# Kernel optimization log

Hardware: AMD Instinct MI355X
Metric: run time of the kernel (lower is better)

## Reference

```python
import jax, jax.numpy as jnp
import numpy as np
from jax.scipy.linalg import expm

B, S, D = 8, 2048, 1024          # batch, seq, input_dim
C, CD = 16, 64                   # num_concepts, concept_dim
L = C * CD                       # latent_dim = 1024
ALPHA, BETA = 0.3, 1.0
LN_EPS = 1e-5                    # torch nn.LayerNorm default


def layer_norm(x, g, b):
    m = jnp.mean(x, axis=-1, keepdims=True)
    v = jnp.mean(jnp.square(x - m), axis=-1, keepdims=True)
    return (x - m) * jax.lax.rsqrt(v + LN_EPS) * g + b


def setup_inputs() -> dict:
    key = jax.random.key(0)
    ks = jax.random.split(key, 8)
    sc = 0.02
    return {
        "x": jax.random.normal(ks[0], (B, S, D), jnp.float32),
        # encoder: Linear(D, 2L) + LayerNorm(2L)
        "enc_w": jax.random.normal(ks[1], (2 * L, D), jnp.float32) * sc,
        "enc_b": jnp.zeros((2 * L,), jnp.float32),
        "enc_g": jnp.ones((2 * L,), jnp.float32),
        "enc_bt": jnp.zeros((2 * L,), jnp.float32),
        # DAG weights [C, C] (torch inits zeros; use small random for non-trivial math)
        "dag_w": jax.random.normal(ks[2], (C, C), jnp.float32) * 0.1,
        # per-concept transforms: Linear(CD,CD) -> LN(CD) -> ReLU -> Linear(CD,CD), stacked over C
        "cw1": jax.random.normal(ks[3], (C, CD, CD), jnp.float32) * sc,
        "cb1": jnp.zeros((C, CD), jnp.float32),
        "cg": jnp.ones((C, CD), jnp.float32),
        "cbt": jnp.zeros((C, CD), jnp.float32),
        "cw2": jax.random.normal(ks[4], (C, CD, CD), jnp.float32) * sc,
        "cb2": jnp.zeros((C, CD), jnp.float32),
        # decoder: Linear(L,L) -> LN(L) -> ReLU -> Linear(L,D)
        "dec_w1": jax.random.normal(ks[5], (L, L), jnp.float32) * sc,
        "dec_b1": jnp.zeros((L,), jnp.float32),
        "dec_g": jnp.ones((L,), jnp.float32),
        "dec_bt": jnp.zeros((L,), jnp.float32),
        "dec_w2": jax.random.normal(ks[6], (D, L), jnp.float32) * sc,
        "dec_b2": jnp.zeros((D,), jnp.float32),
    }


def reference(x, enc_w, enc_b, enc_g, enc_bt, dag_w, cw1, cb1, cg, cbt, cw2, cb2,
              dec_w1, dec_b1, dec_g, dec_bt, dec_w2, dec_b2):
    # ---- encode ----
    h = layer_norm(jnp.einsum('bsd,kd->bsk', x, enc_w) + enc_b, enc_g, enc_bt)  # [B,S,2L]
    mu, logvar = jnp.split(h, 2, axis=-1)                                        # [B,S,L] each
    z = mu  # eval-mode reparameterize

    # ---- causal transform ----
    zc = z.reshape(B, S, C, CD)                                   # [B,S,C,CD]
    dag = jnp.tril(jax.nn.softplus(dag_w), k=-1)                  # [C,C]
    z_causal = zc + jnp.einsum('ij,bsjd->bsid', dag, zc)          # [B,S,C,CD]

    # per-concept Linear -> LN -> ReLU -> Linear, batched over concept axis
    t = jnp.einsum('bsce,cde->bscd', z_causal, cw1) + cb1         # [B,S,C,CD]
    t = layer_norm(t, cg, cbt)
    t = jax.nn.relu(t)
    t = jnp.einsum('bsce,cde->bscd', t, cw2) + cb2
    z_t = t.reshape(B, S, L)

    # ---- decode ----
    d = layer_norm(jnp.einsum('bsl,kl->bsk', z_t, dec_w1) + dec_b1, dec_g, dec_bt)
    d = jax.nn.relu(d)
    x_recon = jnp.einsum('bsl,dl->bsd', d, dec_w2) + dec_b2        # [B,S,D]

    # ---- losses ----
    recon_loss = jnp.mean(jnp.square(x_recon - x))
    kl_loss = -0.5 * jnp.mean(1.0 + logvar - jnp.square(mu) - jnp.exp(logvar))
    dag_loss = jnp.sum(jnp.abs(dag)) + jnp.trace(expm(dag))
    total_loss = recon_loss + ALPHA * kl_loss + BETA * dag_loss
    return x_recon, total_loss, kl_loss, recon_loss, dag_loss
```

## Files before the change

kernel.cpp:

```cpp
#include <hip/hip_runtime.h>
#include <stdint.h>


#define NTOK   16384
#define DIM    1024
#define NC     16
#define CD     64
#define NOUT_ELEMS 16777216

typedef float f32x4 __attribute__((ext_vector_type(4)));
typedef __bf16 bf16x8 __attribute__((ext_vector_type(8)));
typedef unsigned short u16x4 __attribute__((ext_vector_type(4)));
typedef unsigned short u16x8 __attribute__((ext_vector_type(8)));

__device__ float g_scal[3];
__device__ float g_part[512];

__device__ __forceinline__ float b2f(uint16_t u) {
  union { uint32_t i; float f; } v; v.i = ((uint32_t)u) << 16; return v.f;
}
__device__ __forceinline__ uint16_t f2b(float f) {
  union { float f; uint32_t i; } v; v.f = f;
  uint32_t x = v.i;
  return (uint16_t)((x + 0x7fffu + ((x >> 16) & 1u)) >> 16);
}

__device__ __forceinline__ void gload_lds16(const uint16_t* g, uint16_t* l) {
  __builtin_amdgcn_global_load_lds(
      (const __attribute__((address_space(1))) void*)g,
      (__attribute__((address_space(3))) void*)l, 16, 0, 0);
}

__device__ __forceinline__ void cvt8(const float* s, uint16_t* d) {
  const f32x4 a = *(const f32x4*)s;
  const f32x4 b = *(const f32x4*)(s + 4);
  u16x8 o;
  o[0]=f2b(a[0]); o[1]=f2b(a[1]); o[2]=f2b(a[2]); o[3]=f2b(a[3]);
  o[4]=f2b(b[0]); o[5]=f2b(b[1]); o[6]=f2b(b[2]); o[7]=f2b(b[3]);
  *(u16x8*)d = o;
}

__global__ __launch_bounds__(256) void cvt_x_kernel(
    const float* __restrict__ src, uint16_t* __restrict__ dst)
{
  const int i = blockIdx.x * 256 + threadIdx.x;
  cvt8(src + (size_t)i * 8, dst + (size_t)i * 8);
}

__global__ __launch_bounds__(256) void cvt_weights_kernel(
    const float* __restrict__ ew, const float* __restrict__ d1,
    const float* __restrict__ d2, const float* __restrict__ c1,
    const float* __restrict__ c2, uint16_t* __restrict__ out)
{
  const int i = blockIdx.x * 256 + threadIdx.x;
  const float* src; uint16_t* dst; int off;
  if (i < 262144)      { src = ew; dst = out;           off = i; }
  else if (i < 393216) { src = d1; dst = out + 2097152; off = i - 262144; }
  else if (i < 524288) { src = d2; dst = out + 3145728; off = i - 393216; }
  else if (i < 532480) { src = c1; dst = out + 4194304; off = i - 524288; }
  else                 { src = c2; dst = out + 4259840; off = i - 532480; }
  cvt8(src + (size_t)off * 8, dst + (size_t)off * 8);
}

__device__ __forceinline__ void stage_half(
    const uint16_t* __restrict__ G, uint16_t* L, int h, int lda,
    int sr, int pc, int wave)
{
#pragma unroll
  for (int i = 0; i < 2; ++i) {
    const int r = h * 128 + i * 64 + sr;
    gload_lds16(G + (size_t)r * lda + (size_t)((pc ^ (sr & 7)) * 8),
                (uint16_t*)((char*)L + h * 16384 + i * 8192 + wave * 1024));
  }
}

template<typename TC, bool SPLIT, bool RECON>
__global__ __launch_bounds__(512, 2) void gemm256_kernel(
    const uint16_t* __restrict__ A, const uint16_t* __restrict__ Wm,
    const float* __restrict__ bias, TC* __restrict__ C0, TC* __restrict__ C1,
    const float* __restrict__ Xref,
    int K, int lda, int ldw, int ldc)
{
  __shared__ __align__(16) uint16_t lds[65536];

  const int tid  = threadIdx.x;
  const int wave = tid >> 6;
  const int lane = tid & 63;
  const int q    = lane >> 4;
  const int r16  = lane & 15;
  const int wm   = wave >> 2;
  const int wn   = wave & 3;
  const int sr   = tid >> 3;
  const int pc   = tid & 7;

  const int gx  = gridDim.x;
  const int gy  = gridDim.y;
  const int nwg = gx * gy;
  const int o   = blockIdx.y * gx + blockIdx.x;
  const int w   = (o & 7) * (nwg >> 3) + (o >> 3);
  const int bn  = (w & (gy - 1)) * 256;
  const int bm  = (w >> __builtin_ctz(gy)) * 256;

  const uint16_t* Ab = A  + (size_t)bm * lda;
  const uint16_t* Wb = Wm + (size_t)bn * ldw;

  const int T = K >> 6;

  stage_half(Ab,      lds,                 0, lda, sr, pc, wave);
  stage_half(Ab,      lds,                 1, lda, sr, pc, wave);
  stage_half(Wb,      lds + 16384,         0, ldw, sr, pc, wave);
  stage_half(Wb,      lds + 16384,         1, ldw, sr, pc, wave);
  if (T > 1) {
    stage_half(Wb + 64, lds + 32768 + 16384, 0, ldw, sr, pc, wave);
    stage_half(Wb + 64, lds + 32768 + 16384, 1, ldw, sr, pc, wave);
    asm volatile("s_waitcnt vmcnt(4)" ::: "memory");
  } else {
    asm volatile("s_waitcnt vmcnt(0)" ::: "memory");
  }
  __builtin_amdgcn_s_barrier();

  f32x4 acc[8][4] = {};
  const int cxa = r16 & 7;
  const int c0  = (q ^ cxa) * 8;
  const int c1  = ((4 + q) ^ cxa) * 8;

  for (int t = 0; t < T; ++t) {
    uint16_t* As  = lds + (t & 1) * 32768;
    uint16_t* Bs  = As + 16384;
    uint16_t* Asn = lds + ((t & 1) ^ 1) * 32768;

    const uint16_t* a_rd = As + (wm * 128 + r16) * 64;
    const uint16_t* b_rd = Bs + (wn * 64  + r16) * 64;

    bf16x8 bfr[4][2], af0[2][2];
#pragma unroll
    for (int ni = 0; ni < 4; ++ni) {
      bfr[ni][0] = *(const bf16x8*)(b_rd + ni * 1024 + c0);
      bfr[ni][1] = *(const bf16x8*)(b_rd + ni * 1024 + c1);
    }
#pragma unroll
    for (int mi2 = 0; mi2 < 2; ++mi2) {
      af0[mi2][0] = *(const bf16x8*)(a_rd + mi2 * 1024 + c0);
      af0[mi2][1] = *(const bf16x8*)(a_rd + mi2 * 1024 + c1);
    }
    if (t + 1 < T) {
      stage_half(Ab + (size_t)(t + 1) * 64, Asn, 0, lda, sr, pc, wave);
      stage_half(Ab + (size_t)(t + 1) * 64, Asn, 1, lda, sr, pc, wave);
    }
    asm volatile("s_waitcnt lgkmcnt(0)" ::: "memory");
    __builtin_amdgcn_s_barrier();
    if (t + 2 < T) {
      stage_half(Wb + (size_t)(t + 2) * 64, Bs, 0, ldw, sr, pc, wave);
      stage_half(Wb + (size_t)(t + 2) * 64, Bs, 1, ldw, sr, pc, wave);
    }

    __builtin_amdgcn_s_setprio(1);
#pragma unroll
    for (int ks = 0; ks < 2; ++ks)
#pragma unroll
      for (int mi2 = 0; mi2 < 2; ++mi2)
#pragma unroll
        for (int ni = 0; ni < 4; ++ni)
          acc[mi2][ni] = __builtin_amdgcn_mfma_f32_16x16x32_bf16(
              af0[mi2][ks], bfr[ni][ks], acc[mi2][ni], 0, 0, 0);

    bf16x8 aP0 = *(const bf16x8*)(a_rd + 2 * 1024 + c0);
    bf16x8 aP1 = *(const bf16x8*)(a_rd + 2 * 1024 + c1);
#pragma unroll
    for (int mi = 2; mi < 8; ++mi) {
      const bf16x8 a0 = aP0, a1 = aP1;
      if (mi < 7) {
        aP0 = *(const bf16x8*)(a_rd + (mi + 1) * 1024 + c0);
        aP1 = *(const bf16x8*)(a_rd + (mi + 1) * 1024 + c1);
      }
#pragma unroll
      for (int ni = 0; ni < 4; ++ni)
        acc[mi][ni] = __builtin_amdgcn_mfma_f32_16x16x32_bf16(
            a0, bfr[ni][0], acc[mi][ni], 0, 0, 0);
#pragma unroll
      for (int ni = 0; ni < 4; ++ni)
        acc[mi][ni] = __builtin_amdgcn_mfma_f32_16x16x32_bf16(
            a1, bfr[ni][1], acc[mi][ni], 0, 0, 0);
    }
    __builtin_amdgcn_s_setprio(0);

    if (t + 2 < T)      asm volatile("s_waitcnt vmcnt(4)" ::: "memory");
    else if (t + 1 < T) asm volatile("s_waitcnt vmcnt(0)" ::: "memory");
    __builtin_amdgcn_s_barrier();
  }

  TC* Cq = C0;
  int cb = bn;
  if constexpr (SPLIT) {
    if (bn >= 1024) { Cq = C1; cb = bn - 1024; }
  }
  float bv[4];
#pragma unroll
  for (int ni = 0; ni < 4; ++ni) bv[ni] = bias[bn + wn * 64 + ni * 16 + r16];

  float rsum = 0.f;
#pragma unroll
  for (int mi = 0; mi < 8; ++mi) {
    const int rbase = bm + wm * 128 + mi * 16 + q * 4;
#pragma unroll
    for (int r = 0; r < 4; ++r) {
      const size_t rowoff = (size_t)(rbase + r) * ldc + cb;
#pragma unroll
      for (int ni = 0; ni < 4; ++ni) {
        const int loc = wn * 64 + ni * 16 + r16;
        const float v = acc[mi][ni][r] + bv[ni];
        if constexpr (sizeof(TC) == 2)
          Cq[rowoff + loc] = f2b(v);
        else
          Cq[rowoff + loc] = v;
        if constexpr (RECON) {
          const float dd = v - Xref[rowoff + loc];
          rsum += dd * dd;
        }
      }
    }
  }
  if constexpr (RECON) {
#pragma unroll
    for (int m = 1; m < 64; m <<= 1) rsum += __shfl_xor(rsum, m);
    __shared__ float redR[8];
    if (lane == 0) redR[wave] = rsum;
    __syncthreads();
    if (tid == 0) {
      float s = 0.f;
#pragma unroll
      for (int w2 = 0; w2 < 8; ++w2) s += redR[w2];
      atomicAdd(&g_part[256 + (w & 255)], s);
    }
  }
}

__global__ __launch_bounds__(256) void concept_fused_kernel(
    uint16_t* __restrict__ z, const uint16_t* __restrict__ c1b,
    const uint16_t* __restrict__ c2b, const float* __restrict__ cb1,
    const float* __restrict__ cg, const float* __restrict__ cbt,
    const float* __restrict__ cb2)
{
  __shared__ __align__(16) uint16_t Az[128 * 64];
  __shared__ __align__(16) uint16_t W1s[64 * 64];
  __shared__ __align__(16) uint16_t W2s[64 * 64];

  const int tid  = threadIdx.x;
  const int wave = tid >> 6;
  const int lane = tid & 63;
  const int q    = lane >> 4;
  const int r16  = lane & 15;
  const int c    = blockIdx.y;
  const int m0   = blockIdx.x * 128;

  const int lr = tid >> 3;
  const int pc = tid & 7;

#pragma unroll
  for (int i = 0; i < 4; ++i) {
    const int r = i * 32 + lr;
    const int gc = pc ^ (r & 7);
    gload_lds16(z + (size_t)(m0 + r) * DIM + c * 64 + gc * 8,
                (uint16_t*)((char*)Az + i * 4096 + wave * 1024));
  }
#pragma unroll
  for (int i = 0; i < 2; ++i) {
    const int r = i * 32 + lr;
    const int gc = pc ^ (r & 7);
    gload_lds16(c1b + (size_t)c * 4096 + r * 64 + gc * 8,
                (uint16_t*)((char*)W1s + i * 4096 + wave * 1024));
    gload_lds16(c2b + (size_t)c * 4096 + r * 64 + gc * 8,
                (uint16_t*)((char*)W2s + i * 4096 + wave * 1024));
  }
  __syncthreads();

  f32x4 acc[2][4] = {};
#pragma unroll
  for (int ks = 0; ks < 2; ++ks) {
    bf16x8 af[2], wf[4];
#pragma unroll
    for (int mi = 0; mi < 2; ++mi) {
      const int row = wave * 32 + mi * 16 + r16;
      af[mi] = *(const bf16x8*)(Az + row * 64 + ((ks * 4 + q) ^ (row & 7)) * 8);
    }
#pragma unroll
    for (int ni = 0; ni < 4; ++ni) {
      const int d = ni * 16 + r16;
      wf[ni] = *(const bf16x8*)(W1s + d * 64 + ((ks * 4 + q) ^ (d & 7)) * 8);
    }
#pragma unroll
    for (int mi = 0; mi < 2; ++mi)
#pragma unroll
      for (int ni = 0; ni < 4; ++ni)
        acc[mi][ni] = __builtin_amdgcn_mfma_f32_16x16x32_bf16(
            af[mi], wf[ni], acc[mi][ni], 0, 0, 0);
  }

  float b1v[4], cgv[4], cbv[4], b2v[4];
#pragma unroll
  for (int ni = 0; ni < 4; ++ni) {
    const int cn = ni * 16 + r16;
    b1v[ni] = cb1[c * 64 + cn];
    cgv[ni] = cg[c * 64 + cn];
    cbv[ni] = cbt[c * 64 + cn];
    b2v[ni] = cb2[c * 64 + cn];
  }
#pragma unroll
  for (int mi = 0; mi < 2; ++mi) {
#pragma unroll
    for (int r = 0; r < 4; ++r) {
      float s1 = 0.f, s2 = 0.f;
#pragma unroll
      for (int ni = 0; ni < 4; ++ni) {
        const float v = acc[mi][ni][r] + b1v[ni];
        acc[mi][ni][r] = v;
        s1 += v; s2 += v * v;
      }
#pragma unroll
      for (int m = 1; m < 16; m <<= 1) {
        s1 += __shfl_xor(s1, m);
        s2 += __shfl_xor(s2, m);
      }
      const float mean = s1 * (1.f / 64.f);
      const float var  = s2 * (1.f / 64.f) - mean * mean;
      const float rs   = rsqrtf(var + 1e-5f);
      const int row = wave * 32 + mi * 16 + q * 4 + r;
#pragma unroll
      for (int ni = 0; ni < 4; ++ni) {
        const float y = fmaxf((acc[mi][ni][r] - mean) * rs * cgv[ni] + cbv[ni], 0.f);
        const int cn = ni * 16 + r16;
        Az[row * 64 + (((cn >> 3) ^ (row & 7)) * 8) + (cn & 7)] = f2b(y);
      }
    }
  }
  __syncthreads();

  f32x4 acc2[2][4] = {};
#pragma unroll
  for (int ks = 0; ks < 2; ++ks) {
    bf16x8 af[2], wf[4];
#pragma unroll
    for (int mi = 0; mi < 2; ++mi) {
      const int row = wave * 32 + mi * 16 + r16;
      af[mi] = *(const bf16x8*)(Az + row * 64 + ((ks * 4 + q) ^ (row & 7)) * 8);
    }
#pragma unroll
    for (int ni = 0; ni < 4; ++ni) {
      const int d = ni * 16 + r16;
      wf[ni] = *(const bf16x8*)(W2s + d * 64 + ((ks * 4 + q) ^ (d & 7)) * 8);
    }
#pragma unroll
    for (int mi = 0; mi < 2; ++mi)
#pragma unroll
      for (int ni = 0; ni < 4; ++ni)
        acc2[mi][ni] = __builtin_amdgcn_mfma_f32_16x16x32_bf16(
            af[mi], wf[ni], acc2[mi][ni], 0, 0, 0);
  }

#pragma unroll
  for (int mi = 0; mi < 2; ++mi)
#pragma unroll
    for (int ni = 0; ni < 4; ++ni) {
      const int cn = ni * 16 + r16;
#pragma unroll
      for (int r = 0; r < 4; ++r) {
        const int row = wave * 32 + mi * 16 + q * 4 + r;
        z[(size_t)(m0 + row) * DIM + c * 64 + cn] = f2b(acc2[mi][ni][r] + b2v[ni]);
      }
    }
}

__global__ __launch_bounds__(256) void kl_causal_kernel(
    const uint16_t* __restrict__ lv, uint16_t* __restrict__ mu,
    const float* __restrict__ g, const float* __restrict__ b,
    const float* __restrict__ dag_w)
{
  __shared__ __align__(16) float zsh[1024];
  __shared__ float dg[256];
  __shared__ float red[8];
  __shared__ float red2[4];
  const int tid = threadIdx.x;
  const int tok = blockIdx.x;
  const int e0  = tid * 4;

  {
    const int di = tid >> 4, dj = tid & 15;
    dg[tid] = (dj < di) ? log1pf(expf(dag_w[tid])) : 0.f;
  }

  const uint16_t* lvp = lv + (size_t)tok * 1024;
  uint16_t*       mup = mu + (size_t)tok * 1024;

  const u16x4 m4 = *(const u16x4*)(mup + e0);
  const u16x4 l4 = *(const u16x4*)(lvp + e0);
  float xm[4], xl[4];
  float s1 = 0.f, s2 = 0.f;
#pragma unroll
  for (int k = 0; k < 4; ++k) {
    xm[k] = b2f(m4[k]);
    xl[k] = b2f(l4[k]);
    s1 += xm[k] + xl[k];
    s2 += xm[k] * xm[k] + xl[k] * xl[k];
  }
#pragma unroll
  for (int m = 1; m < 64; m <<= 1) {
    s1 += __shfl_xor(s1, m);
    s2 += __shfl_xor(s2, m);
  }
  const int wave = tid >> 6, lane = tid & 63;
  if (lane == 0) { red[wave] = s1; red[4 + wave] = s2; }
  __syncthreads();
  s1 = red[0] + red[1] + red[2] + red[3];
  s2 = red[4] + red[5] + red[6] + red[7];
  const float mean = s1 * (1.f / 2048.f);
  const float var  = s2 * (1.f / 2048.f) - mean * mean;
  const float rs   = rsqrtf(var + 1e-5f);

  const f32x4 g4m = *(const f32x4*)(g + e0);
  const f32x4 b4m = *(const f32x4*)(b + e0);
  const f32x4 g4l = *(const f32x4*)(g + 1024 + e0);
  const f32x4 b4l = *(const f32x4*)(b + 1024 + e0);
  float kl = 0.f;
  f32x4 z;
#pragma unroll
  for (int k = 0; k < 4; ++k) {
    z[k] = (xm[k] - mean) * rs * g4m[k] + b4m[k];
    const float y = (xl[k] - mean) * rs * g4l[k] + b4l[k];
    kl += 1.f + y - z[k] * z[k] - expf(y);
  }
  *(f32x4*)(zsh + e0) = z;
#pragma unroll
  for (int m = 1; m < 64; m <<= 1) kl += __shfl_xor(kl, m);
  if (lane == 0) red2[wave] = kl;
  __syncthreads();
  if (tid == 0)
    atomicAdd(&g_part[tok & 255], red2[0] + red2[1] + red2[2] + red2[3]);

  const int i  = e0 >> 6;
  const int d0 = e0 & 63;
  f32x4 s = *(const f32x4*)(zsh + e0);
  for (int j = 0; j < i; ++j) {
    const float w = dg[i * 16 + j];
    const f32x4 zj = *(const f32x4*)(zsh + j * 64 + d0);
    s[0] += w * zj[0]; s[1] += w * zj[1]; s[2] += w * zj[2]; s[3] += w * zj[3];
  }
  u16x4 o;
#pragma unroll
  for (int k = 0; k < 4; ++k) o[k] = f2b(s[k]);
  *(u16x4*)(mup + e0) = o;
}

__global__ __launch_bounds__(256) void ln_relu_kernel(
    uint16_t* __restrict__ data, const float* __restrict__ g,
    const float* __restrict__ b)
{
  const int tid = threadIdx.x;
  const int e0  = tid * 4;
  uint16_t* p = data + (size_t)blockIdx.x * 1024;

  const u16x4 v4 = *(const u16x4*)(p + e0);
  float x[4];
  float s1 = 0.f, s2 = 0.f;
#pragma unroll
  for (int k = 0; k < 4; ++k) {
    x[k] = b2f(v4[k]);
    s1 += x[k];
    s2 += x[k] * x[k];
  }
#pragma unroll
  for (int m = 1; m < 64; m <<= 1) {
    s1 += __shfl_xor(s1, m);
    s2 += __shfl_xor(s2, m);
  }
  __shared__ float red[8];
  const int wave = tid >> 6, lane = tid & 63;
  if (lane == 0) { red[wave] = s1; red[4 + wave] = s2; }
  __syncthreads();
  s1 = red[0] + red[1] + red[2] + red[3];
  s2 = red[4] + red[5] + red[6] + red[7];
  const float mean = s1 * (1.f / 1024.f);
  const float var  = s2 * (1.f / 1024.f) - mean * mean;
  const float rs   = rsqrtf(var + 1e-5f);

  const f32x4 g4 = *(const f32x4*)(g + e0);
  const f32x4 b4 = *(const f32x4*)(b + e0);
  u16x4 o;
#pragma unroll
  for (int k = 0; k < 4; ++k) {
    const float y = (x[k] - mean) * rs * g4[k] + b4[k];
    o[k] = f2b(fmaxf(y, 0.f));
  }
  *(u16x4*)(p + e0) = o;
}

__global__ __launch_bounds__(256) void dag_init_kernel(
    const float* __restrict__ dag_w)
{
  const int t = threadIdx.x;
  g_part[t] = 0.f;
  g_part[256 + t] = 0.f;
  const int i = t >> 4, j = t & 15;
  const float v = (j < i) ? log1pf(expf(dag_w[t])) : 0.f;
  float s = v;
#pragma unroll
  for (int m = 1; m < 64; m <<= 1) s += __shfl_xor(s, m);
  __shared__ float red[4];
  const int wave = t >> 6, lane = t & 63;
  if (lane == 0) red[wave] = s;
  __syncthreads();
  if (t == 0)
    g_scal[2] = red[0] + red[1] + red[2] + red[3] + 16.f;
}

__global__ __launch_bounds__(256) void finalize_kernel(float* __restrict__ out_tail)
{
  const int tid = threadIdx.x;
  float kl = g_part[tid];
  float rc = g_part[256 + tid];
#pragma unroll
  for (int m = 1; m < 64; m <<= 1) {
    kl += __shfl_xor(kl, m);
    rc += __shfl_xor(rc, m);
  }
  __shared__ float red[8];
  const int wave = tid >> 6, lane = tid & 63;
  if (lane == 0) { red[wave] = kl; red[4 + wave] = rc; }
  __syncthreads();
  if (tid == 0) {
    const float kls = red[0] + red[1] + red[2] + red[3];
    const float rcs = red[4] + red[5] + red[6] + red[7];
    const float kl_l   = -0.5f * kls * (1.f / (16384.f * 1024.f));
    const float recon  = rcs * (1.f / 16777216.f);
    const float dagl   = g_scal[2];
    out_tail[0] = recon + 0.3f * kl_l + 1.0f * dagl;
    out_tail[1] = kl_l;
    out_tail[2] = recon;
    out_tail[3] = dagl;
  }
}

extern "C" void kernel_launch(void* const* d_in, const int* in_sizes, int n_in,
                              void* d_out, int out_size, void* d_ws, size_t ws_size,
                              hipStream_t stream) {
  const float* x      = (const float*)d_in[0];
  const float* enc_w  = (const float*)d_in[1];
  const float* enc_b  = (const float*)d_in[2];
  const float* enc_g  = (const float*)d_in[3];
  const float* enc_bt = (const float*)d_in[4];
  const float* dag_w  = (const float*)d_in[5];
  const float* cw1    = (const float*)d_in[6];
  const float* cb1    = (const float*)d_in[7];
  const float* cg     = (const float*)d_in[8];
  const float* cbt    = (const float*)d_in[9];
  const float* cw2    = (const float*)d_in[10];
  const float* cb2    = (const float*)d_in[11];
  const float* dec_w1 = (const float*)d_in[12];
  const float* dec_b1 = (const float*)d_in[13];
  const float* dec_g  = (const float*)d_in[14];
  const float* dec_bt = (const float*)d_in[15];
  const float* dec_w2 = (const float*)d_in[16];
  const float* dec_b2 = (const float*)d_in[17];

  uint16_t* S    = (uint16_t*)d_ws;
  uint16_t* Wbf  = (uint16_t*)((char*)d_ws + (size_t)NTOK * DIM * 2);
  uint16_t* ewb  = Wbf;
  uint16_t* d1b  = Wbf + 2097152;
  uint16_t* d2b  = Wbf + 3145728;
  uint16_t* c1b  = Wbf + 4194304;
  uint16_t* c2b  = Wbf + 4259840;

  uint16_t* Obf  = (uint16_t*)d_out;
  uint16_t* xbf  = Obf + (size_t)NOUT_ELEMS;
  float*    O    = (float*)d_out;

  dag_init_kernel<<<1, 256, 0, stream>>>(dag_w);

  cvt_x_kernel<<<NOUT_ELEMS / 8 / 256, 256, 0, stream>>>(x, xbf);
  cvt_weights_kernel<<<2112, 256, 0, stream>>>(enc_w, dec_w1, dec_w2, cw1, cw2, Wbf);

  gemm256_kernel<uint16_t, true, false>
      <<<dim3(64, 8, 1), 512, 0, stream>>>(
      xbf, ewb, enc_b, Obf, S, nullptr, DIM, DIM, DIM, DIM);

  kl_causal_kernel<<<NTOK, 256, 0, stream>>>(S, Obf, enc_g, enc_bt, dag_w);

  concept_fused_kernel<<<dim3(128, 16, 1), 256, 0, stream>>>(
      Obf, c1b, c2b, cb1, cg, cbt, cb2);

  gemm256_kernel<uint16_t, false, false>
      <<<dim3(64, 4, 1), 512, 0, stream>>>(
      Obf, d1b, dec_b1, S, S, nullptr, DIM, DIM, DIM, DIM);

  ln_relu_kernel<<<NTOK, 256, 0, stream>>>(S, dec_g, dec_bt);

  gemm256_kernel<float, false, true>
      <<<dim3(64, 4, 1), 512, 0, stream>>>(
      S, d2b, dec_b2, O, O, x, DIM, DIM, DIM, DIM);

  finalize_kernel<<<1, 256, 0, stream>>>(O + (size_t)NOUT_ELEMS);
}
```

Baseline: 383.0 us.

## Fuse x fp32-to-bf16 conversion into encoder GEMM A-tile staging

The encoder GEMM now reads fp32 x directly, converting to bf16 in registers and writing LDS, which removes the separate cvt_x pass and its bf16 round trip through memory. The dag_init kernel is folded into an extra block of the weight conversion kernel to save a launch. The GEMM pipeline also changes: A and B for the next step are both prefetched at the top of each iteration into the other buffer, replacing the two-deep B prefetch and the mid-iteration barrier. The fp32 A path doubles the A global read bytes and adds conversion and register pressure, and the new schedule exposes more load latency per step in all three GEMMs.

```diff
diff --git a/kernel.cpp b/kernel.cpp
--- a/kernel.cpp
+++ b/kernel.cpp
@@ -40,18 +40,29 @@
   *(u16x8*)d = o;
 }
 
-__global__ __launch_bounds__(256) void cvt_x_kernel(
-    const float* __restrict__ src, uint16_t* __restrict__ dst)
-{
-  const int i = blockIdx.x * 256 + threadIdx.x;
-  cvt8(src + (size_t)i * 8, dst + (size_t)i * 8);
-}
-
 __global__ __launch_bounds__(256) void cvt_weights_kernel(
     const float* __restrict__ ew, const float* __restrict__ d1,
     const float* __restrict__ d2, const float* __restrict__ c1,
-    const float* __restrict__ c2, uint16_t* __restrict__ out)
+    const float* __restrict__ c2, uint16_t* __restrict__ out,
+    const float* __restrict__ dag_w)
 {
+  if (blockIdx.x == 2112) {
+    const int t = threadIdx.x;
+    g_part[t] = 0.f;
+    g_part[256 + t] = 0.f;
+    const int i2 = t >> 4, j2 = t & 15;
+    const float v = (j2 < i2) ? log1pf(expf(dag_w[t])) : 0.f;
+    float s = v;
+#pragma unroll
+    for (int m = 1; m < 64; m <<= 1) s += __shfl_xor(s, m);
+    __shared__ float red[4];
+    const int wave = t >> 6, lane = t & 63;
+    if (lane == 0) red[wave] = s;
+    __syncthreads();
+    if (t == 0)
+      g_scal[2] = red[0] + red[1] + red[2] + red[3] + 16.f;
+    return;
+  }
   const int i = blockIdx.x * 256 + threadIdx.x;
   const float* src; uint16_t* dst; int off;
   if (i < 262144)      { src = ew; dst = out;           off = i; }
@@ -74,13 +85,14 @@
   }
 }
 
-template<typename TC, bool SPLIT, bool RECON>
+template<typename TA, typename TC, bool SPLIT, bool RECON>
 __global__ __launch_bounds__(512, 2) void gemm256_kernel(
-    const uint16_t* __restrict__ A, const uint16_t* __restrict__ Wm,
+    const TA* __restrict__ A, const uint16_t* __restrict__ Wm,
     const float* __restrict__ bias, TC* __restrict__ C0, TC* __restrict__ C1,
     const float* __restrict__ Xref,
     int K, int lda, int ldw, int ldc)
 {
+  constexpr bool CVTA = (sizeof(TA) == 4);
   __shared__ __align__(16) uint16_t lds[65536];
 
   const int tid  = threadIdx.x;
@@ -101,20 +113,37 @@
   const int bn  = (w & (gy - 1)) * 256;
   const int bm  = (w >> __builtin_ctz(gy)) * 256;
 
-  const uint16_t* Ab = A  + (size_t)bm * lda;
-  const uint16_t* Wb = Wm + (size_t)bn * ldw;
+  const TA*       Abase = A  + (size_t)bm * lda;
+  const uint16_t* Wb    = Wm + (size_t)bn * ldw;
 
   const int T = K >> 6;
 
-  stage_half(Ab,      lds,                 0, lda, sr, pc, wave);
-  stage_half(Ab,      lds,                 1, lda, sr, pc, wave);
-  stage_half(Wb,      lds + 16384,         0, ldw, sr, pc, wave);
-  stage_half(Wb,      lds + 16384,         1, ldw, sr, pc, wave);
-  if (T > 1) {
-    stage_half(Wb + 64, lds + 32768 + 16384, 0, ldw, sr, pc, wave);
-    stage_half(Wb + 64, lds + 32768 + 16384, 1, ldw, sr, pc, wave);
+  if constexpr (CVTA) {
+    f32x4 pLo[4], pHi[4];
+#pragma unroll
+    for (int j = 0; j < 4; ++j) {
+      const int r = j * 64 + sr;
+      const float* src = (const float*)Abase + (size_t)r * lda + (pc ^ (r & 7)) * 8;
+      pLo[j] = *(const f32x4*)src;
+      pHi[j] = *(const f32x4*)(src + 4);
+    }
+    stage_half(Wb, lds + 16384, 0, ldw, sr, pc, wave);
+    stage_half(Wb, lds + 16384, 1, ldw, sr, pc, wave);
     asm volatile("s_waitcnt vmcnt(4)" ::: "memory");
+#pragma unroll
+    for (int j = 0; j < 4; ++j) {
+      const int r = j * 64 + sr;
+      bf16x8 ov;
+#pragma unroll
+      for (int e = 0; e < 4; ++e) { ov[e] = (__bf16)pLo[j][e]; ov[4 + e] = (__bf16)pHi[j][e]; }
+      *(bf16x8*)(lds + r * 64 + pc * 8) = ov;
+    }
+    asm volatile("s_waitcnt vmcnt(0) lgkmcnt(0)" ::: "memory");
   } else {
+    stage_half((const uint16_t*)Abase, lds, 0, lda, sr, pc, wave);
+    stage_half((const uint16_t*)Abase, lds, 1, lda, sr, pc, wave);
+    stage_half(Wb, lds + 16384, 0, ldw, sr, pc, wave);
+    stage_half(Wb, lds + 16384, 1, ldw, sr, pc, wave);
     asm volatile("s_waitcnt vmcnt(0)" ::: "memory");
   }
   __builtin_amdgcn_s_barrier();
@@ -128,6 +157,27 @@
     uint16_t* As  = lds + (t & 1) * 32768;
     uint16_t* Bs  = As + 16384;
     uint16_t* Asn = lds + ((t & 1) ^ 1) * 32768;
+    uint16_t* Bsn = Asn + 16384;
+    const bool pf = (t + 1 < T);
+
+    f32x4 aLo[4], aHi[4];
+    if (pf) {
+      if constexpr (CVTA) {
+#pragma unroll
+        for (int j = 0; j < 4; ++j) {
+          const int r = j * 64 + sr;
+          const float* src = (const float*)Abase + (size_t)r * lda
+                           + (t + 1) * 64 + (pc ^ (r & 7)) * 8;
+          aLo[j] = *(const f32x4*)src;
+          aHi[j] = *(const f32x4*)(src + 4);
+        }
+      } else {
+        stage_half((const uint16_t*)Abase + (size_t)(t + 1) * 64, Asn, 0, lda, sr, pc, wave);
+        stage_half((const uint16_t*)Abase + (size_t)(t + 1) * 64, Asn, 1, lda, sr, pc, wave);
+      }
+      stage_half(Wb + (size_t)(t + 1) * 64, Bsn, 0, ldw, sr, pc, wave);
+      stage_half(Wb + (size_t)(t + 1) * 64, Bsn, 1, ldw, sr, pc, wave);
+    }
 
     const uint16_t* a_rd = As + (wm * 128 + r16) * 64;
     const uint16_t* b_rd = Bs + (wn * 64  + r16) * 64;
@@ -142,16 +192,6 @@
     for (int mi2 = 0; mi2 < 2; ++mi2) {
       af0[mi2][0] = *(const bf16x8*)(a_rd + mi2 * 1024 + c0);
       af0[mi2][1] = *(const bf16x8*)(a_rd + mi2 * 1024 + c1);
-    }
-    if (t + 1 < T) {
-      stage_half(Ab + (size_t)(t + 1) * 64, Asn, 0, lda, sr, pc, wave);
-      stage_half(Ab + (size_t)(t + 1) * 64, Asn, 1, lda, sr, pc, wave);
-    }
-    asm volatile("s_waitcnt lgkmcnt(0)" ::: "memory");
-    __builtin_amdgcn_s_barrier();
-    if (t + 2 < T) {
-      stage_half(Wb + (size_t)(t + 2) * 64, Bs, 0, ldw, sr, pc, wave);
-      stage_half(Wb + (size_t)(t + 2) * 64, Bs, 1, ldw, sr, pc, wave);
     }
 
     __builtin_amdgcn_s_setprio(1);
@@ -184,8 +224,22 @@
     }
     __builtin_amdgcn_s_setprio(0);
 
-    if (t + 2 < T)      asm volatile("s_waitcnt vmcnt(4)" ::: "memory");
-    else if (t + 1 < T) asm volatile("s_waitcnt vmcnt(0)" ::: "memory");
+    if (pf) {
+      if constexpr (CVTA) {
+        asm volatile("s_waitcnt vmcnt(4)" ::: "memory");
+#pragma unroll
+        for (int j = 0; j < 4; ++j) {
+          const int r = j * 64 + sr;
+          bf16x8 ov;
+#pragma unroll
+          for (int e = 0; e < 4; ++e) { ov[e] = (__bf16)aLo[j][e]; ov[4 + e] = (__bf16)aHi[j][e]; }
+          *(bf16x8*)(Asn + r * 64 + pc * 8) = ov;
+        }
+        asm volatile("s_waitcnt vmcnt(0) lgkmcnt(0)" ::: "memory");
+      } else {
+        asm volatile("s_waitcnt vmcnt(0)" ::: "memory");
+      }
+    }
     __builtin_amdgcn_s_barrier();
   }
 
@@ -491,25 +545,6 @@
     o[k] = f2b(fmaxf(y, 0.f));
   }
   *(u16x4*)(p + e0) = o;
-}
-
-__global__ __launch_bounds__(256) void dag_init_kernel(
-    const float* __restrict__ dag_w)
-{
-  const int t = threadIdx.x;
-  g_part[t] = 0.f;
-  g_part[256 + t] = 0.f;
-  const int i = t >> 4, j = t & 15;
-  const float v = (j < i) ? log1pf(expf(dag_w[t])) : 0.f;
-  float s = v;
-#pragma unroll
-  for (int m = 1; m < 64; m <<= 1) s += __shfl_xor(s, m);
-  __shared__ float red[4];
-  const int wave = t >> 6, lane = t & 63;
-  if (lane == 0) red[wave] = s;
-  __syncthreads();
-  if (t == 0)
-    g_scal[2] = red[0] + red[1] + red[2] + red[3] + 16.f;
 }
 
 __global__ __launch_bounds__(256) void finalize_kernel(float* __restrict__ out_tail)
@@ -570,30 +605,27 @@
   uint16_t* c2b  = Wbf + 4259840;
 
   uint16_t* Obf  = (uint16_t*)d_out;
-  uint16_t* xbf  = Obf + (size_t)NOUT_ELEMS;
   float*    O    = (float*)d_out;
 
-  dag_init_kernel<<<1, 256, 0, stream>>>(dag_w);
-
-  cvt_x_kernel<<<NOUT_ELEMS / 8 / 256, 256, 0, stream>>>(x, xbf);
-  cvt_weights_kernel<<<2112, 256, 0, stream>>>(enc_w, dec_w1, dec_w2, cw1, cw2, Wbf);
-
-  gemm256_kernel<uint16_t, true, false>
+  cvt_weights_kernel<<<2113, 256, 0, stream>>>(
+      enc_w, dec_w1, dec_w2, cw1, cw2, Wbf, dag_w);
+
+  gemm256_kernel<float, uint16_t, true, false>
       <<<dim3(64, 8, 1), 512, 0, stream>>>(
-      xbf, ewb, enc_b, Obf, S, nullptr, DIM, DIM, DIM, DIM);
+      x, ewb, enc_b, Obf, S, nullptr, DIM, DIM, DIM, DIM);
 
   kl_causal_kernel<<<NTOK, 256, 0, stream>>>(S, Obf, enc_g, enc_bt, dag_w);
 
   concept_fused_kernel<<<dim3(128, 16, 1), 256, 0, stream>>>(
       Obf, c1b, c2b, cb1, cg, cbt, cb2);
 
-  gemm256_kernel<uint16_t, false, false>
+  gemm256_kernel<uint16_t, uint16_t, false, false>
       <<<dim3(64, 4, 1), 512, 0, stream>>>(
       Obf, d1b, dec_b1, S, S, nullptr, DIM, DIM, DIM, DIM);
 
   ln_relu_kernel<<<NTOK, 256, 0, stream>>>(S, dec_g, dec_bt);
 
-  gemm256_kernel<float, false, true>
+  gemm256_kernel<uint16_t, float, false, true>
       <<<dim3(64, 4, 1), 512, 0, stream>>>(
       S, d2b, dec_b2, O, O, x, DIM, DIM, DIM, DIM);
 
```

Result: no change. 385.9 us (+0.7%).
